# Performance work log

Measured on AMD Instinct MI355X. Metric: run time of the kernel, lower is better.

Reference implementation:

```python
import jax, jax.numpy as jnp
import numpy as np

THRESHOLD = 1.0
DECAY = 0.9
SURR_SLOPE = 10.0

B, T, IN, HID, OUT = 1024, 16, 2312, 1024, 10


def setup_inputs() -> dict:
    key = jax.random.key(0)
    kx, kw1, kb1, kw2, kb2 = jax.random.split(key, 5)
    x = jax.random.normal(kx, (B, T, IN), dtype=jnp.float32)
    # PyTorch nn.Linear default init: U(-1/sqrt(fan_in), 1/sqrt(fan_in))
    lim1 = 1.0 / np.sqrt(IN)
    lim2 = 1.0 / np.sqrt(HID)
    W1 = jax.random.uniform(kw1, (HID, IN), jnp.float32, -lim1, lim1)
    b1 = jax.random.uniform(kb1, (HID,), jnp.float32, -lim1, lim1)
    W2 = jax.random.uniform(kw2, (OUT, HID), jnp.float32, -lim2, lim2)
    b2 = jax.random.uniform(kb2, (OUT,), jnp.float32, -lim2, lim2)
    return {"x": x, "W1": W1, "b1": b1, "W2": W2, "b2": b2}


def _lif_step(v, inp):
    # leaky integrate-and-fire with sigmoid surrogate spike
    v_new = DECAY * v + inp
    spike = jax.nn.sigmoid(SURR_SLOPE * (v_new - THRESHOLD))
    v_next = v_new * (1.0 - spike)
    return v_next, spike


def reference(x, W1, b1, W2, b2):
    # x: [B, T, IN] -> spikes: [B, T, OUT]
    Bn = x.shape[0]
    v1_0 = jnp.zeros((Bn, W1.shape[0]), x.dtype)
    v2_0 = jnp.zeros((Bn, W2.shape[0]), x.dtype)

    # Precompute the first linear over all time steps (batched GEMM).
    h_all = jnp.einsum('bti,hi->bth', x, W1) + b1  # [B, T, HID]

    def step(carry, h_t):
        v1, v2 = carry
        v1, s1 = _lif_step(v1, h_t)                 # [B, HID]
        o_t = s1 @ W2.T + b2                        # [B, OUT]
        v2, s2 = _lif_step(v2, o_t)
        return (v1, v2), s2

    h_tb = jnp.swapaxes(h_all, 0, 1)                # [T, B, HID]
    _, spikes = jax.lax.scan(step, (v1_0, v2_0), h_tb)
    return jnp.swapaxes(spikes, 0, 1)               # [B, T, OUT]
```

## Files before the change

kernel.cpp:

```cpp
#include <hip/hip_runtime.h>

typedef _Float16 half8  __attribute__((ext_vector_type(8)));
typedef _Float16 half4v __attribute__((ext_vector_type(4)));
typedef float    floatx4 __attribute__((ext_vector_type(4)));

#define K_DIM 2312
#define KP    2368
#define N_DIM 1024
#define M_DIM 16384
#define T_DIM 16
#define O_DIM 10
#define NKT   73
#define NT_OLD 73
#define LDP 40

__global__ __launch_bounds__(256) void cvt_f32_f16_pad(const float* __restrict__ src,
                                                       _Float16* __restrict__ dst) {
  int row = blockIdx.x;
  const float* s = src + (size_t)row * K_DIM;
  _Float16* d = dst + (size_t)row * KP;
  for (int c = threadIdx.x; c < 296; c += 256) {
    half8 o;
    if (c < 289) {
      floatx4 a = *(const floatx4*)(s + c * 8);
      floatx4 b = *(const floatx4*)(s + c * 8 + 4);
      #pragma unroll
      for (int e = 0; e < 4; ++e) { o[e] = (_Float16)a[e]; o[4 + e] = (_Float16)b[e]; }
    } else {
      o = half8{0, 0, 0, 0, 0, 0, 0, 0};
    }
    *(half8*)(d + c * 8) = o;
  }
}

__device__ __forceinline__ void gload16(const _Float16* g, _Float16* l) {
  __builtin_amdgcn_global_load_lds((const __attribute__((address_space(1))) void*)g,
                                   (__attribute__((address_space(3))) void*)l, 16, 0, 0);
}

__device__ __forceinline__ half8 cvt8(floatx4 a, floatx4 b) {
  half8 r;
  #pragma unroll
  for (int e = 0; e < 4; ++e) { r[e] = (_Float16)a[e]; r[4 + e] = (_Float16)b[e]; }
  return r;
}

__device__ __forceinline__ half8 cvt8_masked(floatx4 a, floatx4 b, int kbase) {
  half8 r;
  #pragma unroll
  for (int e = 0; e < 4; ++e) {
    r[e]     = (kbase + e     < K_DIM) ? (_Float16)a[e] : (_Float16)0.f;
    r[4 + e] = (kbase + 4 + e < K_DIM) ? (_Float16)b[e] : (_Float16)0.f;
  }
  return r;
}

__global__ __launch_bounds__(512, 2) void gemm_fused(const float* __restrict__ X,
                                                     const _Float16* __restrict__ Bw,
                                                     const float* __restrict__ b1,
                                                     float* __restrict__ h) {
  __shared__ __align__(16) _Float16 As[2][256 * 32];
  __shared__ __align__(16) _Float16 Bs[3][256 * 32];

  const int tid  = threadIdx.x;
  const int lane = tid & 63;
  const int w    = tid >> 6;
  const int wm   = (w >> 2) * 128;
  const int wn   = (w & 3) * 64;
  const int bm   = blockIdx.x & 63;
  const int bn   = blockIdx.x >> 6;
  const int m0   = bm * 256;
  const int n0   = bn * 256;

  const int rA   = tid >> 1;
  const int kA   = (tid & 1) * 16;
  const int keyA = (rA >> 1) & 3;
  const int gA   = kA >> 3;
  const float* xa = X + (size_t)(m0 + rA) * K_DIM;
  const int dstA0 = rA * 32 + ((gA    ) ^ keyA) * 8;
  const int dstA1 = rA * 32 + ((gA + 1) ^ keyA) * 8;

  const int rlo  = lane >> 2;
  const int keyB = (rlo >> 1) & 3;
  const int cch  = (lane & 3) ^ keyB;
  const _Float16* bg = Bw + (size_t)(n0 + w * 32 + rlo) * KP + cch * 8;
  const int stbB = (w * 32) * 32;

  floatx4 acc[8][4];
  #pragma unroll
  for (int i = 0; i < 8; ++i)
    #pragma unroll
    for (int j = 0; j < 4; ++j)
      acc[i][j] = floatx4{0.f, 0.f, 0.f, 0.f};

  const int fr  = lane & 15;
  const int g   = lane >> 4;
  const int rds = (g ^ ((fr >> 1) & 3)) * 8;
  int offA[8], offB[4];
  #pragma unroll
  for (int i = 0; i < 8; ++i) offA[i] = (wm + i * 16 + fr) * 32 + rds;
  #pragma unroll
  for (int j = 0; j < 4; ++j) offB[j] = (wn + j * 16 + fr) * 32 + rds;

  half8 af[8], bf[4];
  floatx4 L0, L1, M0v, M1v;

#define CLAMPK(k) ((k) > (K_DIM - 4) ? (K_DIM - 4) : (k))
#define LOADL(ts) do { int _k = (ts) * 32 + kA;                              \
    L0  = *(const floatx4*)(xa + CLAMPK(_k));                                \
    L1  = *(const floatx4*)(xa + CLAMPK(_k + 4)); } while (0)
#define LOADM(ts) do { int _k = (ts) * 32 + kA + 8;                          \
    M0v = *(const floatx4*)(xa + CLAMPK(_k));                                \
    M1v = *(const floatx4*)(xa + CLAMPK(_k + 4)); } while (0)
#define STAGEB(ts) do { const int _s = (ts) % 3;                             \
    gload16(bg + (ts) * 32,           &Bs[_s][stbB]);                        \
    gload16(bg + (ts) * 32 + 16 * KP, &Bs[_s][stbB + 16 * 32]); } while (0)

#define READF(tk) do {                                                       \
    const _Float16* _A = As[(tk) & 1];                                       \
    const _Float16* _B = Bs[(tk) % 3];                                       \
    _Pragma("unroll")                                                        \
    for (int _i = 0; _i < 8; ++_i) af[_i] = *(const half8*)(&_A[offA[_i]]);  \
    _Pragma("unroll")                                                        \
    for (int _j = 0; _j < 4; ++_j) bf[_j] = *(const half8*)(&_B[offB[_j]]);  \
  } while (0)

#define MFMA32 do {                                                          \
    __builtin_amdgcn_s_setprio(1);                                           \
    _Pragma("unroll")                                                        \
    for (int _i = 0; _i < 8; ++_i)                                           \
      _Pragma("unroll")                                                      \
      for (int _j = 0; _j < 4; ++_j)                                         \
        acc[_i][_j] = __builtin_amdgcn_mfma_f32_16x16x32_f16(af[_i], bf[_j], acc[_i][_j], 0, 0, 0); \
    __builtin_amdgcn_s_setprio(0);                                           \
  } while (0)

  LOADL(0); LOADM(0);
  asm volatile("s_waitcnt vmcnt(0)" ::: "memory");
  __builtin_amdgcn_sched_barrier(0);
  *(half8*)(&As[0][dstA0]) = cvt8(L0, L1);
  *(half8*)(&As[0][dstA1]) = cvt8(M0v, M1v);
  STAGEB(0);
  LOADL(1); LOADM(1);
  STAGEB(1);
  asm volatile("s_waitcnt vmcnt(0)" ::: "memory");
  __builtin_amdgcn_sched_barrier(0);
  asm volatile("s_waitcnt lgkmcnt(0)" ::: "memory");
  __builtin_amdgcn_sched_barrier(0);
  __builtin_amdgcn_s_barrier();
  __builtin_amdgcn_sched_barrier(0);
  READF(0);

  for (int t = 0; t < NKT - 2; ++t) {
    const int wsl = (t + 1) & 1;
    asm volatile("s_waitcnt vmcnt(4)" ::: "memory");
    __builtin_amdgcn_sched_barrier(0);
    *(half8*)(&As[wsl][dstA0]) = cvt8(L0, L1);
    LOADL(t + 2);
    __builtin_amdgcn_sched_barrier(0);
    asm volatile("s_waitcnt vmcnt(4)" ::: "memory");
    __builtin_amdgcn_sched_barrier(0);
    *(half8*)(&As[wsl][dstA1]) = cvt8(M0v, M1v);
    LOADM(t + 2);
    STAGEB(t + 2);
    __builtin_amdgcn_sched_barrier(0);
    asm volatile("s_waitcnt vmcnt(6)" ::: "memory");
    __builtin_amdgcn_sched_barrier(0);
    asm volatile("s_waitcnt lgkmcnt(0)" ::: "memory");
    __builtin_amdgcn_sched_barrier(0);
    __builtin_amdgcn_s_barrier();
    __builtin_amdgcn_sched_barrier(0);
    MFMA32;
    READF(t + 1);
  }

  {
    const int kb = (NKT - 1) * 32 + kA;
    asm volatile("s_waitcnt vmcnt(4)" ::: "memory");
    __builtin_amdgcn_sched_barrier(0);
    *(half8*)(&As[(NKT - 1) & 1][dstA0]) = cvt8_masked(L0, L1, kb);
    asm volatile("s_waitcnt vmcnt(2)" ::: "memory");
    __builtin_amdgcn_sched_barrier(0);
    *(half8*)(&As[(NKT - 1) & 1][dstA1]) = cvt8_masked(M0v, M1v, kb + 8);
    asm volatile("s_waitcnt vmcnt(0)" ::: "memory");
    __builtin_amdgcn_sched_barrier(0);
    asm volatile("s_waitcnt lgkmcnt(0)" ::: "memory");
    __builtin_amdgcn_sched_barrier(0);
    __builtin_amdgcn_s_barrier();
    __builtin_amdgcn_sched_barrier(0);
    MFMA32;
    READF(NKT - 1);
  }
  MFMA32;

#undef CLAMPK
#undef LOADL
#undef LOADM
#undef STAGEB
#undef READF
#undef MFMA32

  const int cr = (lane >> 4) * 4;
  #pragma unroll
  for (int j = 0; j < 4; ++j) {
    int col = n0 + wn + j * 16 + fr;
    float bv = b1[col];
    #pragma unroll
    for (int i = 0; i < 8; ++i) {
      int rbase = m0 + wm + i * 16 + cr;
      #pragma unroll
      for (int e = 0; e < 4; ++e)
        h[(size_t)(rbase + e) * N_DIM + col] = acc[i][j][e] + bv;
    }
  }
}

__device__ __forceinline__ void stage_load(const float* __restrict__ x,
                                           const float* __restrict__ w,
                                           int m0, int n0, int k0, int tid,
                                           floatx4 (&ar)[4], floatx4 (&br)[4]) {
  int r = tid >> 3;
  int c = (tid & 7) * 4;
  bool ok = (k0 + c) < K_DIM;
  #pragma unroll
  for (int i = 0; i < 4; ++i) {
    int row = r + 32 * i;
    if (ok) {
      ar[i] = *(const floatx4*)(x + (size_t)(m0 + row) * K_DIM + k0 + c);
      br[i] = *(const floatx4*)(w + (size_t)(n0 + row) * K_DIM + k0 + c);
    } else {
      ar[i] = floatx4{0.f, 0.f, 0.f, 0.f};
      br[i] = floatx4{0.f, 0.f, 0.f, 0.f};
    }
  }
}

__device__ __forceinline__ void stage_write(_Float16* __restrict__ Ab,
                                            _Float16* __restrict__ Bb, int tid,
                                            const floatx4 (&ar)[4], const floatx4 (&br)[4]) {
  int r = tid >> 3;
  int c = (tid & 7) * 4;
  #pragma unroll
  for (int i = 0; i < 4; ++i) {
    int row = r + 32 * i;
    half4v av, bv;
    #pragma unroll
    for (int e = 0; e < 4; ++e) {
      av[e] = (_Float16)ar[i][e];
      bv[e] = (_Float16)br[i][e];
    }
    *(half4v*)(Ab + row * LDP + c) = av;
    *(half4v*)(Bb + row * LDP + c) = bv;
  }
}

__global__ __launch_bounds__(256) void gemm1_kernel(const float* __restrict__ x,
                                                    const float* __restrict__ W1,
                                                    const float* __restrict__ b1,
                                                    float* __restrict__ h) {
  __shared__ _Float16 Al[2][128 * LDP];
  __shared__ _Float16 Bl[2][128 * LDP];

  int tid  = threadIdx.x;
  int lane = tid & 63;
  int w    = tid >> 6;
  int wm   = (w >> 1) * 64;
  int wn   = (w & 1) * 64;
  int m0   = (blockIdx.x >> 3) * 128;
  int n0   = (blockIdx.x & 7) * 128;

  floatx4 acc[4][4];
  #pragma unroll
  for (int i = 0; i < 4; ++i)
    #pragma unroll
    for (int j = 0; j < 4; ++j)
      acc[i][j] = floatx4{0.f, 0.f, 0.f, 0.f};

  floatx4 ar[4], br[4];
  stage_load(x, W1, m0, n0, 0, tid, ar, br);
  stage_write(Al[0], Bl[0], tid, ar, br);
  __syncthreads();

  int fr = lane & 15;
  int kc = (lane >> 4) * 8;

  int cur = 0;
  for (int kt = 0; kt < NT_OLD; ++kt) {
    if (kt + 1 < NT_OLD) stage_load(x, W1, m0, n0, (kt + 1) * 32, tid, ar, br);

    const _Float16* Ab = Al[cur];
    const _Float16* Bb = Bl[cur];
    half8 af[4], bf[4];
    #pragma unroll
    for (int f = 0; f < 4; ++f) {
      af[f] = *(const half8*)(Ab + (wm + f * 16 + fr) * LDP + kc);
      bf[f] = *(const half8*)(Bb + (wn + f * 16 + fr) * LDP + kc);
    }
    #pragma unroll
    for (int i = 0; i < 4; ++i)
      #pragma unroll
      for (int j = 0; j < 4; ++j)
        acc[i][j] = __builtin_amdgcn_mfma_f32_16x16x32_f16(af[i], bf[j], acc[i][j], 0, 0, 0);

    if (kt + 1 < NT_OLD) stage_write(Al[cur ^ 1], Bl[cur ^ 1], tid, ar, br);
    __syncthreads();
    cur ^= 1;
  }

  int cr = (lane >> 4) * 4;
  #pragma unroll
  for (int j = 0; j < 4; ++j) {
    int col = n0 + wn + j * 16 + fr;
    float bv = b1[col];
    #pragma unroll
    for (int i = 0; i < 4; ++i) {
      int rbase = m0 + wm + i * 16 + cr;
      #pragma unroll
      for (int e = 0; e < 4; ++e)
        h[(size_t)(rbase + e) * N_DIM + col] = acc[i][j][e] + bv;
    }
  }
}

__global__ __launch_bounds__(256) void snn_temporal_kernel(const float* __restrict__ h,
                                                           const float* __restrict__ W2,
                                                           const float* __restrict__ b2,
                                                           float* __restrict__ out) {
  __shared__ float w2s[O_DIM * N_DIM];
  int tid = threadIdx.x;
  for (int i = tid; i < O_DIM * N_DIM; i += 256) w2s[i] = W2[i];
  __syncthreads();

  int wave = tid >> 6;
  int lane = tid & 63;
  int b = blockIdx.x * 4 + wave;
  const float* hrow = h + (size_t)b * (T_DIM * N_DIM);
  float* orow = out + (size_t)b * (T_DIM * O_DIM);

  float v1[16];
  #pragma unroll
  for (int e = 0; e < 16; ++e) v1[e] = 0.f;
  float v2 = 0.f;
  float bias2 = (lane < O_DIM) ? b2[lane] : 0.f;

  floatx4 hv[4];
  #pragma unroll
  for (int c = 0; c < 4; ++c) hv[c] = *(const floatx4*)(hrow + c * 256 + lane * 4);

  for (int t = 0; t < T_DIM; ++t) {
    floatx4 hn[4];
    if (t + 1 < T_DIM) {
      #pragma unroll
      for (int c = 0; c < 4; ++c)
        hn[c] = *(const floatx4*)(hrow + (t + 1) * N_DIM + c * 256 + lane * 4);
    }

    float sarr[16];
    #pragma unroll
    for (int c = 0; c < 4; ++c) {
      #pragma unroll
      for (int e = 0; e < 4; ++e) {
        int ii = c * 4 + e;
        float vn = 0.9f * v1[ii] + hv[c][e];
        float s  = 1.f / (1.f + __expf(10.f - 10.f * vn));
        v1[ii] = vn * (1.f - s);
        sarr[ii] = s;
      }
    }

    float part[10];
    #pragma unroll
    for (int o = 0; o < O_DIM; ++o) {
      float a = 0.f;
      #pragma unroll
      for (int c = 0; c < 4; ++c) {
        floatx4 w4 = *(const floatx4*)&w2s[o * N_DIM + c * 256 + lane * 4];
        a += sarr[c * 4 + 0] * w4[0] + sarr[c * 4 + 1] * w4[1]
           + sarr[c * 4 + 2] * w4[2] + sarr[c * 4 + 3] * w4[3];
      }
      part[o] = a;
    }
    #pragma unroll
    for (int m = 1; m < 64; m <<= 1) {
      #pragma unroll
      for (int o = 0; o < O_DIM; ++o) part[o] += __shfl_xor(part[o], m, 64);
    }

    float po = part[0];
    #pragma unroll
    for (int o = 1; o < O_DIM; ++o) po = (lane == o) ? part[o] : po;

    if (lane < O_DIM) {
      float vo = 0.9f * v2 + po + bias2;
      float s2 = 1.f / (1.f + __expf(10.f - 10.f * vo));
      v2 = vo * (1.f - s2);
      orow[t * O_DIM + lane] = s2;
    }

    #pragma unroll
    for (int c = 0; c < 4; ++c) hv[c] = hn[c];
  }
}

extern "C" void kernel_launch(void* const* d_in, const int* in_sizes, int n_in,
                              void* d_out, int out_size, void* d_ws, size_t ws_size,
                              hipStream_t stream) {
  const float* x  = (const float*)d_in[0];
  const float* W1 = (const float*)d_in[1];
  const float* b1 = (const float*)d_in[2];
  const float* W2 = (const float*)d_in[3];
  const float* b2 = (const float*)d_in[4];
  float* out = (float*)d_out;

  float* h = (float*)d_ws;

  const size_t H_BYTES  = (size_t)M_DIM * N_DIM * 4;
  const size_t WH_BYTES = (size_t)N_DIM * KP * 2;
  const size_t NEED = H_BYTES + WH_BYTES;

  if (ws_size >= NEED) {
    _Float16* w1h = (_Float16*)((char*)d_ws + H_BYTES);
    cvt_f32_f16_pad<<<dim3(N_DIM), dim3(256), 0, stream>>>(W1, w1h);
    gemm_fused<<<dim3(256), dim3(512), 0, stream>>>(x, w1h, b1, h);
  } else {
    gemm1_kernel<<<dim3(1024), dim3(256), 0, stream>>>(x, W1, b1, h);
  }
  snn_temporal_kernel<<<dim3(256), dim3(256), 0, stream>>>(h, W2, b2, out);
}
```

Before: 143.5 us.

## Triple-buffer A tiles and deepen GEMM prefetch pipeline

Expands the shared-memory A buffer from two to three stages and restructures the main K-loop so the fp32 X loads run one tile further ahead. The converted A tile and the B tile are now written two iterations before use, and the waitcnt/barrier placement is rewritten accordingly. The aim is to hide global-load latency and to drop the split wait in the middle of each iteration. The cost is more LDS per block (six 16 KB buffers), which may limit residency at two blocks per CU, plus riskier hand-tuned lgkmcnt counts.

```diff
diff --git a/kernel.cpp b/kernel.cpp
--- a/kernel.cpp
+++ b/kernel.cpp
@@ -55,11 +55,15 @@
   return r;
 }
 
-__global__ __launch_bounds__(512, 2) void gemm_fused(const float* __restrict__ X,
-                                                     const _Float16* __restrict__ Bw,
-                                                     const float* __restrict__ b1,
-                                                     float* __restrict__ h) {
-  __shared__ __align__(16) _Float16 As[2][256 * 32];
+#define VMCNT(n)  asm volatile("s_waitcnt vmcnt(" #n ")" ::: "memory")
+#define LGKM(n)   asm volatile("s_waitcnt lgkmcnt(" #n ")" ::: "memory")
+#define SBAR      __builtin_amdgcn_sched_barrier(0)
+
+__global__ __launch_bounds__(512, 2) void gemm_fused2(const float* __restrict__ X,
+                                                      const _Float16* __restrict__ Bw,
+                                                      const float* __restrict__ b1,
+                                                      float* __restrict__ h) {
+  __shared__ __align__(16) _Float16 As[3][256 * 32];
   __shared__ __align__(16) _Float16 Bs[3][256 * 32];
 
   const int tid  = threadIdx.x;
@@ -112,19 +116,24 @@
 #define LOADM(ts) do { int _k = (ts) * 32 + kA + 8;                          \
     M0v = *(const floatx4*)(xa + CLAMPK(_k));                                \
     M1v = *(const floatx4*)(xa + CLAMPK(_k + 4)); } while (0)
+#define WRITEA(ts) do { _Float16* _d = As[(ts) % 3];                         \
+    *(half8*)(&_d[dstA0]) = cvt8(L0, L1);                                    \
+    *(half8*)(&_d[dstA1]) = cvt8(M0v, M1v); } while (0)
+#define WRITEA_MASK(ts) do { _Float16* _d = As[(ts) % 3];                    \
+    const int _kb = (ts) * 32 + kA;                                          \
+    *(half8*)(&_d[dstA0]) = cvt8_masked(L0, L1, _kb);                        \
+    *(half8*)(&_d[dstA1]) = cvt8_masked(M0v, M1v, _kb + 8); } while (0)
 #define STAGEB(ts) do { const int _s = (ts) % 3;                             \
     gload16(bg + (ts) * 32,           &Bs[_s][stbB]);                        \
     gload16(bg + (ts) * 32 + 16 * KP, &Bs[_s][stbB + 16 * 32]); } while (0)
-
 #define READF(tk) do {                                                       \
-    const _Float16* _A = As[(tk) & 1];                                       \
+    const _Float16* _A = As[(tk) % 3];                                       \
     const _Float16* _B = Bs[(tk) % 3];                                       \
     _Pragma("unroll")                                                        \
     for (int _i = 0; _i < 8; ++_i) af[_i] = *(const half8*)(&_A[offA[_i]]);  \
     _Pragma("unroll")                                                        \
     for (int _j = 0; _j < 4; ++_j) bf[_j] = *(const half8*)(&_B[offB[_j]]);  \
   } while (0)
-
 #define MFMA32 do {                                                          \
     __builtin_amdgcn_s_setprio(1);                                           \
     _Pragma("unroll")                                                        \
@@ -136,66 +145,50 @@
   } while (0)
 
   LOADL(0); LOADM(0);
-  asm volatile("s_waitcnt vmcnt(0)" ::: "memory");
-  __builtin_amdgcn_sched_barrier(0);
-  *(half8*)(&As[0][dstA0]) = cvt8(L0, L1);
-  *(half8*)(&As[0][dstA1]) = cvt8(M0v, M1v);
-  STAGEB(0);
+  VMCNT(0); SBAR;
+  WRITEA(0);
   LOADL(1); LOADM(1);
-  STAGEB(1);
-  asm volatile("s_waitcnt vmcnt(0)" ::: "memory");
-  __builtin_amdgcn_sched_barrier(0);
-  asm volatile("s_waitcnt lgkmcnt(0)" ::: "memory");
-  __builtin_amdgcn_sched_barrier(0);
-  __builtin_amdgcn_s_barrier();
-  __builtin_amdgcn_sched_barrier(0);
+  VMCNT(0); SBAR;
+  WRITEA(1);
+  STAGEB(0); STAGEB(1);
+  LOADL(2); LOADM(2);
+  VMCNT(4); SBAR;
+  LGKM(0);  SBAR;
+  __builtin_amdgcn_s_barrier(); SBAR;
   READF(0);
 
-  for (int t = 0; t < NKT - 2; ++t) {
-    const int wsl = (t + 1) & 1;
-    asm volatile("s_waitcnt vmcnt(4)" ::: "memory");
-    __builtin_amdgcn_sched_barrier(0);
-    *(half8*)(&As[wsl][dstA0]) = cvt8(L0, L1);
-    LOADL(t + 2);
-    __builtin_amdgcn_sched_barrier(0);
-    asm volatile("s_waitcnt vmcnt(4)" ::: "memory");
-    __builtin_amdgcn_sched_barrier(0);
-    *(half8*)(&As[wsl][dstA1]) = cvt8(M0v, M1v);
-    LOADM(t + 2);
+  for (int t = 0; t < NKT - 3; ++t) {
+    VMCNT(0); SBAR;
+    WRITEA(t + 2);
+    LOADL(t + 3); LOADM(t + 3);
     STAGEB(t + 2);
-    __builtin_amdgcn_sched_barrier(0);
-    asm volatile("s_waitcnt vmcnt(6)" ::: "memory");
-    __builtin_amdgcn_sched_barrier(0);
-    asm volatile("s_waitcnt lgkmcnt(0)" ::: "memory");
-    __builtin_amdgcn_sched_barrier(0);
-    __builtin_amdgcn_s_barrier();
-    __builtin_amdgcn_sched_barrier(0);
+    LGKM(14); SBAR;
+    __builtin_amdgcn_s_barrier(); SBAR;
     MFMA32;
     READF(t + 1);
   }
 
-  {
-    const int kb = (NKT - 1) * 32 + kA;
-    asm volatile("s_waitcnt vmcnt(4)" ::: "memory");
-    __builtin_amdgcn_sched_barrier(0);
-    *(half8*)(&As[(NKT - 1) & 1][dstA0]) = cvt8_masked(L0, L1, kb);
-    asm volatile("s_waitcnt vmcnt(2)" ::: "memory");
-    __builtin_amdgcn_sched_barrier(0);
-    *(half8*)(&As[(NKT - 1) & 1][dstA1]) = cvt8_masked(M0v, M1v, kb + 8);
-    asm volatile("s_waitcnt vmcnt(0)" ::: "memory");
-    __builtin_amdgcn_sched_barrier(0);
-    asm volatile("s_waitcnt lgkmcnt(0)" ::: "memory");
-    __builtin_amdgcn_sched_barrier(0);
-    __builtin_amdgcn_s_barrier();
-    __builtin_amdgcn_sched_barrier(0);
-    MFMA32;
-    READF(NKT - 1);
-  }
+  VMCNT(0); SBAR;
+  WRITEA_MASK(NKT - 1);
+  STAGEB(NKT - 1);
+  LGKM(14); SBAR;
+  __builtin_amdgcn_s_barrier(); SBAR;
+  MFMA32;
+  READF(NKT - 2);
+
+  VMCNT(0); SBAR;
+  LGKM(12); SBAR;
+  __builtin_amdgcn_s_barrier(); SBAR;
+  MFMA32;
+  READF(NKT - 1);
+
   MFMA32;
 
 #undef CLAMPK
 #undef LOADL
 #undef LOADM
+#undef WRITEA
+#undef WRITEA_MASK
 #undef STAGEB
 #undef READF
 #undef MFMA32
@@ -421,7 +414,7 @@
   if (ws_size >= NEED) {
     _Float16* w1h = (_Float16*)((char*)d_ws + H_BYTES);
     cvt_f32_f16_pad<<<dim3(N_DIM), dim3(256), 0, stream>>>(W1, w1h);
-    gemm_fused<<<dim3(256), dim3(512), 0, stream>>>(x, w1h, b1, h);
+    gemm_fused2<<<dim3(256), dim3(512), 0, stream>>>(x, w1h, b1, h);
   } else {
     gemm1_kernel<<<dim3(1024), dim3(256), 0, stream>>>(x, W1, b1, h);
   }
```

After: 142.9 us. No clear change (-0.4%).
